# Kernel tuning notes

Hardware: AMD Instinct MI355X
Metric: run time of the kernel (lower is better)

## Reference

```python
import jax, jax.numpy as jnp
import numpy as np

B, L, D = 64, 4096, 512

def setup_inputs() -> dict:
    key = jax.random.key(0)
    k1, k2 = jax.random.split(key)
    current_hidden = jax.random.normal(k1, (B, D), dtype=jnp.float32)
    encoder_outputs = jax.random.normal(k2, (B, L, D), dtype=jnp.float32)
    return {"current_hidden": current_hidden, "encoder_outputs": encoder_outputs}

def reference(current_hidden, encoder_outputs):
    # energy[b, l] = <current_hidden[b], encoder_outputs[b, l]>  (fused batched matmul,
    # replacing the per-timestep python loop of tiny bmms)
    energy = jnp.einsum('bd,bld->bl', current_hidden, encoder_outputs)
    # softmax over the source-length axis (nn.Softmax(dim=1))
    alignment = jax.nn.softmax(energy, axis=1)  # [B, L]
    # context = mean over L of alignment[..., None] * encoder_outputs
    # (original uses torch.mean, i.e. weighted sum divided by L)
    L_ = encoder_outputs.shape[1]
    context = jnp.einsum('bl,bld->bd', alignment, encoder_outputs) / L_
    return context
```

## Files before the change

### kernel.cpp

```cpp
#include <hip/hip_runtime.h>
#include <hip/hip_bf16.h>


#define D_DIM 512
#define B_DIM 64
#define L_DIM 4096

__global__ __launch_bounds__(256) void attn_pass1(
    const float* __restrict__ h,
    const float* __restrict__ enc,
    float* __restrict__ part_ms,
    float* __restrict__ part_ctx,
    int Cblk)
{
    const int b    = blockIdx.y;
    const int c    = blockIdx.x;
    const int tid  = threadIdx.x;
    const int wave = tid >> 6;
    const int lane = tid & 63;

    const int rowsPerBlock = L_DIM / Cblk;
    const int rowsPerWave  = rowsPerBlock >> 2;
    const int l0 = c * rowsPerBlock + wave * rowsPerWave;

    const float4* h4 = reinterpret_cast<const float4*>(h + (size_t)b * D_DIM);
    const float4 h0 = h4[lane];
    const float4 h1 = h4[lane + 64];

    const float* rowp = enc + ((size_t)b * L_DIM + (size_t)l0) * D_DIM + 4 * lane;

    float m = -3.0e38f;
    float s = 0.0f;
    float4 a0 = {0.f, 0.f, 0.f, 0.f};
    float4 a1 = {0.f, 0.f, 0.f, 0.f};

    float4 v0 = *reinterpret_cast<const float4*>(rowp);
    float4 v1 = *reinterpret_cast<const float4*>(rowp + 256);

    for (int r = 0; r < rowsPerWave; ++r) {
        const float* np = rowp + ((r + 1 < rowsPerWave) ? D_DIM : 0);
        const float4 nv0 = *reinterpret_cast<const float4*>(np);
        const float4 nv1 = *reinterpret_cast<const float4*>(np + 256);

        float e = h0.x * v0.x + h0.y * v0.y + h0.z * v0.z + h0.w * v0.w
                + h1.x * v1.x + h1.y * v1.y + h1.z * v1.z + h1.w * v1.w;
        #pragma unroll
        for (int off = 32; off > 0; off >>= 1)
            e += __shfl_xor(e, off, 64);
        if (e > m) {
            const float alpha = __expf(m - e);
            s *= alpha;
            a0.x *= alpha; a0.y *= alpha; a0.z *= alpha; a0.w *= alpha;
            a1.x *= alpha; a1.y *= alpha; a1.z *= alpha; a1.w *= alpha;
            m = e;
        }
        const float w = __expf(e - m);
        s += w;
        a0.x += w * v0.x; a0.y += w * v0.y; a0.z += w * v0.z; a0.w += w * v0.w;
        a1.x += w * v1.x; a1.y += w * v1.y; a1.z += w * v1.z; a1.w += w * v1.w;

        v0 = nv0; v1 = nv1;
        rowp += D_DIM;
    }

    __shared__ float sm_m[4];
    __shared__ float sm_s[4];
    __shared__ float sm_ctx[4][D_DIM];

    reinterpret_cast<float4*>(&sm_ctx[wave][0])[lane]   = a0;
    reinterpret_cast<float4*>(&sm_ctx[wave][256])[lane] = a1;
    if (lane == 0) { sm_m[wave] = m; sm_s[wave] = s; }
    __syncthreads();

    const float M  = fmaxf(fmaxf(sm_m[0], sm_m[1]), fmaxf(sm_m[2], sm_m[3]));
    const float w0 = __expf(sm_m[0] - M);
    const float w1 = __expf(sm_m[1] - M);
    const float w2 = __expf(sm_m[2] - M);
    const float w3 = __expf(sm_m[3] - M);

    if (tid == 0) {
        const float S = sm_s[0] * w0 + sm_s[1] * w1 + sm_s[2] * w2 + sm_s[3] * w3;
        float* ms = part_ms + ((size_t)b * Cblk + c) * 2;
        ms[0] = M;
        ms[1] = S;
    }

    float* dst = part_ctx + ((size_t)b * Cblk + c) * D_DIM;
    for (int d = tid; d < D_DIM; d += 256) {
        dst[d] = sm_ctx[0][d] * w0 + sm_ctx[1][d] * w1
               + sm_ctx[2][d] * w2 + sm_ctx[3][d] * w3;
    }
}

__global__ __launch_bounds__(256) void attn_pass2(
    const float* __restrict__ part_ms,
    const float* __restrict__ part_ctx,
    float* __restrict__ out,
    int Cblk, float invL)
{
    const int b   = blockIdx.x;
    const int tid = threadIdx.x;

    __shared__ float w_sm[64];
    __shared__ float invSL;

    if (tid == 0) {
        const float* ms = part_ms + (size_t)b * Cblk * 2;
        float M = -3.0e38f;
        for (int i = 0; i < Cblk; ++i) M = fmaxf(M, ms[2 * i]);
        float S = 0.f;
        for (int i = 0; i < Cblk; ++i) {
            const float w = __expf(ms[2 * i] - M);
            w_sm[i] = w;
            S += w * ms[2 * i + 1];
        }
        invSL = invL / S;
    }
    __syncthreads();

    const float scale = invSL;
    for (int d = tid; d < D_DIM; d += 256) {
        float acc = 0.f;
        for (int i = 0; i < Cblk; ++i)
            acc += w_sm[i] * part_ctx[((size_t)b * Cblk + i) * D_DIM + d];
        out[(size_t)b * D_DIM + d] = acc * scale;
    }
}

extern "C" void kernel_launch(void* const* d_in, const int* in_sizes, int n_in,
                              void* d_out, int out_size, void* d_ws, size_t ws_size,
                              hipStream_t stream) {
    const float* h   = (const float*)d_in[0];
    const float* enc = (const float*)d_in[1];
    float* out = (float*)d_out;

    int C = 16;
    while (C > 1) {
        const size_t need = ((size_t)B_DIM * C * 2 + (size_t)B_DIM * C * D_DIM) * sizeof(float);
        if (need <= ws_size) break;
        C >>= 1;
    }

    float* part_ms  = (float*)d_ws;
    float* part_ctx = part_ms + (size_t)B_DIM * C * 2;

    dim3 grid1(C, B_DIM);
    attn_pass1<<<grid1, 256, 0, stream>>>(h, enc, part_ms, part_ctx, C);
    attn_pass2<<<B_DIM, 256, 0, stream>>>(part_ms, part_ctx, out, C, 1.0f / (float)L_DIM);
}
```

Before: 678.4 us.

## Fuse two-pass attention into one cooperative kernel with grid sync and atomics

Replaces the partial-result pass plus reduction pass with a single cooperative kernel. Each block writes its local max and sum into the output buffer as scratch, grid-syncs, computes a global rescale factor, then has chunk 0 store and the other chunks atomically add their scaled context into the output. This removes the second launch and the workspace round-trip. In exchange it adds three grid-wide barriers and atomic contention, and it includes a single-block-per-batch fallback in case the cooperative launch fails.

```diff
diff --git a/kernel.cpp b/kernel.cpp
--- a/kernel.cpp
+++ b/kernel.cpp
@@ -1,17 +1,24 @@
 #include <hip/hip_runtime.h>
-#include <hip/hip_bf16.h>
+#include <hip/hip_cooperative_groups.h>
+
+namespace cg = cooperative_groups;
 
 
 #define D_DIM 512
 #define B_DIM 64
 #define L_DIM 4096
-
-__global__ __launch_bounds__(256) void attn_pass1(
+#define CCHUNK 16
+
+__device__ __forceinline__ float dot8(const float4 h0, const float4 h1,
+                                      const float4 v0, const float4 v1) {
+    return h0.x * v0.x + h0.y * v0.y + h0.z * v0.z + h0.w * v0.w
+         + h1.x * v1.x + h1.y * v1.y + h1.z * v1.z + h1.w * v1.w;
+}
+
+__global__ __launch_bounds__(256) void attn_fused_coop(
     const float* __restrict__ h,
     const float* __restrict__ enc,
-    float* __restrict__ part_ms,
-    float* __restrict__ part_ctx,
-    int Cblk)
+    float* __restrict__ out)
 {
     const int b    = blockIdx.y;
     const int c    = blockIdx.x;
@@ -19,8 +26,8 @@
     const int wave = tid >> 6;
     const int lane = tid & 63;
 
-    const int rowsPerBlock = L_DIM / Cblk;
-    const int rowsPerWave  = rowsPerBlock >> 2;
+    constexpr int rowsPerBlock = L_DIM / CCHUNK;
+    constexpr int rowsPerWave  = rowsPerBlock / 4;
     const int l0 = c * rowsPerBlock + wave * rowsPerWave;
 
     const float4* h4 = reinterpret_cast<const float4*>(h + (size_t)b * D_DIM);
@@ -42,8 +49,7 @@
         const float4 nv0 = *reinterpret_cast<const float4*>(np);
         const float4 nv1 = *reinterpret_cast<const float4*>(np + 256);
 
-        float e = h0.x * v0.x + h0.y * v0.y + h0.z * v0.z + h0.w * v0.w
-                + h1.x * v1.x + h1.y * v1.y + h1.z * v1.z + h1.w * v1.w;
+        float e = dot8(h0, h1, v0, v1);
         #pragma unroll
         for (int off = 32; off > 0; off >>= 1)
             e += __shfl_xor(e, off, 64);
@@ -72,58 +78,133 @@
     if (lane == 0) { sm_m[wave] = m; sm_s[wave] = s; }
     __syncthreads();
 
-    const float M  = fmaxf(fmaxf(sm_m[0], sm_m[1]), fmaxf(sm_m[2], sm_m[3]));
-    const float w0 = __expf(sm_m[0] - M);
-    const float w1 = __expf(sm_m[1] - M);
-    const float w2 = __expf(sm_m[2] - M);
-    const float w3 = __expf(sm_m[3] - M);
-
+    const float blkM = fmaxf(fmaxf(sm_m[0], sm_m[1]), fmaxf(sm_m[2], sm_m[3]));
+    const float w0 = __expf(sm_m[0] - blkM);
+    const float w1 = __expf(sm_m[1] - blkM);
+    const float w2 = __expf(sm_m[2] - blkM);
+    const float w3 = __expf(sm_m[3] - blkM);
+
+    for (int d = tid; d < D_DIM; d += 256) {
+        sm_ctx[0][d] = sm_ctx[0][d] * w0 + sm_ctx[1][d] * w1
+                     + sm_ctx[2][d] * w2 + sm_ctx[3][d] * w3;
+    }
     if (tid == 0) {
-        const float S = sm_s[0] * w0 + sm_s[1] * w1 + sm_s[2] * w2 + sm_s[3] * w3;
-        float* ms = part_ms + ((size_t)b * Cblk + c) * 2;
-        ms[0] = M;
-        ms[1] = S;
-    }
-
-    float* dst = part_ctx + ((size_t)b * Cblk + c) * D_DIM;
-    for (int d = tid; d < D_DIM; d += 256) {
-        dst[d] = sm_ctx[0][d] * w0 + sm_ctx[1][d] * w1
-               + sm_ctx[2][d] * w2 + sm_ctx[3][d] * w3;
-    }
-}
-
-__global__ __launch_bounds__(256) void attn_pass2(
-    const float* __restrict__ part_ms,
-    const float* __restrict__ part_ctx,
-    float* __restrict__ out,
-    int Cblk, float invL)
+        const float blkS = sm_s[0] * w0 + sm_s[1] * w1 + sm_s[2] * w2 + sm_s[3] * w3;
+        float* scratch = out + (size_t)(b * CCHUNK + c) * 2;
+        scratch[0] = blkM;
+        scratch[1] = blkS;
+    }
+
+    cg::grid_group g = cg::this_grid();
+    g.sync();
+
+    __shared__ float s_scale;
+    if (tid == 0) {
+        float M = -3.0e38f;
+        #pragma unroll
+        for (int i = 0; i < CCHUNK; ++i)
+            M = fmaxf(M, out[(size_t)(b * CCHUNK + i) * 2]);
+        float S = 0.f;
+        #pragma unroll
+        for (int i = 0; i < CCHUNK; ++i)
+            S += out[(size_t)(b * CCHUNK + i) * 2 + 1]
+               * __expf(out[(size_t)(b * CCHUNK + i) * 2] - M);
+        s_scale = __expf(blkM - M) / (S * (float)L_DIM);
+    }
+    __syncthreads();
+    const float scale = s_scale;
+
+    g.sync();
+
+    if (c == 0) {
+        for (int d = tid; d < D_DIM; d += 256)
+            out[(size_t)b * D_DIM + d] = scale * sm_ctx[0][d];
+    }
+    g.sync();
+    if (c != 0) {
+        for (int d = tid; d < D_DIM; d += 256)
+            atomicAdd(&out[(size_t)b * D_DIM + d], scale * sm_ctx[0][d]);
+    }
+}
+
+__global__ __launch_bounds__(1024) void attn_fallback(
+    const float* __restrict__ h,
+    const float* __restrict__ enc,
+    float* __restrict__ out)
 {
-    const int b   = blockIdx.x;
-    const int tid = threadIdx.x;
-
-    __shared__ float w_sm[64];
-    __shared__ float invSL;
-
-    if (tid == 0) {
-        const float* ms = part_ms + (size_t)b * Cblk * 2;
-        float M = -3.0e38f;
-        for (int i = 0; i < Cblk; ++i) M = fmaxf(M, ms[2 * i]);
-        float S = 0.f;
-        for (int i = 0; i < Cblk; ++i) {
-            const float w = __expf(ms[2 * i] - M);
-            w_sm[i] = w;
-            S += w * ms[2 * i + 1];
+    const int b    = blockIdx.x;
+    const int tid  = threadIdx.x;
+    const int wave = tid >> 6;
+    const int lane = tid & 63;
+
+    constexpr int rowsPerWave = L_DIM / 16;
+    const int l0 = wave * rowsPerWave;
+
+    const float4* h4 = reinterpret_cast<const float4*>(h + (size_t)b * D_DIM);
+    const float4 h0 = h4[lane];
+    const float4 h1 = h4[lane + 64];
+
+    const float* rowp = enc + ((size_t)b * L_DIM + (size_t)l0) * D_DIM + 4 * lane;
+
+    float m = -3.0e38f;
+    float s = 0.0f;
+    float4 a0 = {0.f, 0.f, 0.f, 0.f};
+    float4 a1 = {0.f, 0.f, 0.f, 0.f};
+
+    float4 v0 = *reinterpret_cast<const float4*>(rowp);
+    float4 v1 = *reinterpret_cast<const float4*>(rowp + 256);
+
+    for (int r = 0; r < rowsPerWave; ++r) {
+        const float* np = rowp + ((r + 1 < rowsPerWave) ? D_DIM : 0);
+        const float4 nv0 = *reinterpret_cast<const float4*>(np);
+        const float4 nv1 = *reinterpret_cast<const float4*>(np + 256);
+
+        float e = dot8(h0, h1, v0, v1);
+        #pragma unroll
+        for (int off = 32; off > 0; off >>= 1)
+            e += __shfl_xor(e, off, 64);
+        if (e > m) {
+            const float alpha = __expf(m - e);
+            s *= alpha;
+            a0.x *= alpha; a0.y *= alpha; a0.z *= alpha; a0.w *= alpha;
+            a1.x *= alpha; a1.y *= alpha; a1.z *= alpha; a1.w *= alpha;
+            m = e;
         }
-        invSL = invL / S;
-    }
+        const float w = __expf(e - m);
+        s += w;
+        a0.x += w * v0.x; a0.y += w * v0.y; a0.z += w * v0.z; a0.w += w * v0.w;
+        a1.x += w * v1.x; a1.y += w * v1.y; a1.z += w * v1.z; a1.w += w * v1.w;
+
+        v0 = nv0; v1 = nv1;
+        rowp += D_DIM;
+    }
+
+    __shared__ float sm_m[16];
+    __shared__ float sm_s[16];
+    __shared__ float sm_ctx[16][D_DIM];
+
+    reinterpret_cast<float4*>(&sm_ctx[wave][0])[lane]   = a0;
+    reinterpret_cast<float4*>(&sm_ctx[wave][256])[lane] = a1;
+    if (lane == 0) { sm_m[wave] = m; sm_s[wave] = s; }
     __syncthreads();
 
-    const float scale = invSL;
-    for (int d = tid; d < D_DIM; d += 256) {
+    float M = -3.0e38f;
+    #pragma unroll
+    for (int i = 0; i < 16; ++i) M = fmaxf(M, sm_m[i]);
+    float w[16];
+    float S = 0.f;
+    #pragma unroll
+    for (int i = 0; i < 16; ++i) {
+        w[i] = __expf(sm_m[i] - M);
+        S += sm_s[i] * w[i];
+    }
+    const float inv = 1.0f / (S * (float)L_DIM);
+
+    for (int d = tid; d < D_DIM; d += 1024) {
         float acc = 0.f;
-        for (int i = 0; i < Cblk; ++i)
-            acc += w_sm[i] * part_ctx[((size_t)b * Cblk + i) * D_DIM + d];
-        out[(size_t)b * D_DIM + d] = acc * scale;
+        #pragma unroll
+        for (int i = 0; i < 16; ++i) acc += sm_ctx[i][d] * w[i];
+        out[(size_t)b * D_DIM + d] = acc * inv;
     }
 }
 
@@ -134,17 +215,12 @@
     const float* enc = (const float*)d_in[1];
     float* out = (float*)d_out;
 
-    int C = 16;
-    while (C > 1) {
-        const size_t need = ((size_t)B_DIM * C * 2 + (size_t)B_DIM * C * D_DIM) * sizeof(float);
-        if (need <= ws_size) break;
-        C >>= 1;
-    }
-
-    float* part_ms  = (float*)d_ws;
-    float* part_ctx = part_ms + (size_t)B_DIM * C * 2;
-
-    dim3 grid1(C, B_DIM);
-    attn_pass1<<<grid1, 256, 0, stream>>>(h, enc, part_ms, part_ctx, C);
-    attn_pass2<<<B_DIM, 256, 0, stream>>>(part_ms, part_ctx, out, C, 1.0f / (float)L_DIM);
-}
+    void* args[] = { (void*)&h, (void*)&enc, (void*)&out };
+    hipError_t err = hipLaunchCooperativeKernel(
+        reinterpret_cast<const void*>(&attn_fused_coop),
+        dim3(CCHUNK, B_DIM), dim3(256), args, 0, stream);
+
+    if (err != hipSuccess) {
+        attn_fallback<<<B_DIM, 1024, 0, stream>>>(h, enc, out);
+    }
+}
```

Result: slower. 986.7 us (+45.4%).

## Interleave rows across waves and double chunk count for more parallelism

Applied to the files above, without the earlier changes.

Doubles the number of chunks per batch to 32, which makes the first-pass grid twice as large, and adds an occupancy hint to launch bounds. Rows are now assigned to waves with an interleaved stride, so concurrently running waves read adjacent rows instead of contiguous private ranges. The intent is to fill more of the GPU and improve DRAM locality on this memory-bound kernel. The workspace-size fallback is removed, so the code now assumes the workspace always fits 32 partials per batch.

```diff
diff --git a/kernel.cpp b/kernel.cpp
--- a/kernel.cpp
+++ b/kernel.cpp
@@ -1,33 +1,33 @@
 #include <hip/hip_runtime.h>
-#include <hip/hip_bf16.h>
 
 
 #define D_DIM 512
 #define B_DIM 64
 #define L_DIM 4096
+#define C_CHUNK 32
+#define WPB 4
+#define WAVES_PER_B (C_CHUNK * WPB)
+#define ROWS_PER_WAVE (L_DIM / WAVES_PER_B)
 
-__global__ __launch_bounds__(256) void attn_pass1(
+__global__ __launch_bounds__(256, 8) void attn_pass1i(
     const float* __restrict__ h,
     const float* __restrict__ enc,
     float* __restrict__ part_ms,
-    float* __restrict__ part_ctx,
-    int Cblk)
+    float* __restrict__ part_ctx)
 {
     const int b    = blockIdx.y;
     const int c    = blockIdx.x;
     const int tid  = threadIdx.x;
     const int wave = tid >> 6;
     const int lane = tid & 63;
-
-    const int rowsPerBlock = L_DIM / Cblk;
-    const int rowsPerWave  = rowsPerBlock >> 2;
-    const int l0 = c * rowsPerBlock + wave * rowsPerWave;
+    const int g    = c * WPB + wave;
 
     const float4* h4 = reinterpret_cast<const float4*>(h + (size_t)b * D_DIM);
     const float4 h0 = h4[lane];
     const float4 h1 = h4[lane + 64];
 
-    const float* rowp = enc + ((size_t)b * L_DIM + (size_t)l0) * D_DIM + 4 * lane;
+    const float* rowp = enc + ((size_t)b * L_DIM + (size_t)g) * D_DIM + 4 * lane;
+    const size_t rowStride = (size_t)WAVES_PER_B * D_DIM;
 
     float m = -3.0e38f;
     float s = 0.0f;
@@ -37,8 +37,8 @@
     float4 v0 = *reinterpret_cast<const float4*>(rowp);
     float4 v1 = *reinterpret_cast<const float4*>(rowp + 256);
 
-    for (int r = 0; r < rowsPerWave; ++r) {
-        const float* np = rowp + ((r + 1 < rowsPerWave) ? D_DIM : 0);
+    for (int r = 0; r < ROWS_PER_WAVE; ++r) {
+        const float* np = rowp + ((r + 1 < ROWS_PER_WAVE) ? rowStride : 0);
         const float4 nv0 = *reinterpret_cast<const float4*>(np);
         const float4 nv1 = *reinterpret_cast<const float4*>(np + 256);
 
@@ -60,7 +60,7 @@
         a1.x += w * v1.x; a1.y += w * v1.y; a1.z += w * v1.z; a1.w += w * v1.w;
 
         v0 = nv0; v1 = nv1;
-        rowp += D_DIM;
+        rowp += rowStride;
     }
 
     __shared__ float sm_m[4];
@@ -80,12 +80,12 @@
 
     if (tid == 0) {
         const float S = sm_s[0] * w0 + sm_s[1] * w1 + sm_s[2] * w2 + sm_s[3] * w3;
-        float* ms = part_ms + ((size_t)b * Cblk + c) * 2;
+        float* ms = part_ms + ((size_t)b * C_CHUNK + c) * 2;
         ms[0] = M;
         ms[1] = S;
     }
 
-    float* dst = part_ctx + ((size_t)b * Cblk + c) * D_DIM;
+    float* dst = part_ctx + ((size_t)b * C_CHUNK + c) * D_DIM;
     for (int d = tid; d < D_DIM; d += 256) {
         dst[d] = sm_ctx[0][d] * w0 + sm_ctx[1][d] * w1
                + sm_ctx[2][d] * w2 + sm_ctx[3][d] * w3;
@@ -96,20 +96,20 @@
     const float* __restrict__ part_ms,
     const float* __restrict__ part_ctx,
     float* __restrict__ out,
-    int Cblk, float invL)
+    float invL)
 {
     const int b   = blockIdx.x;
     const int tid = threadIdx.x;
 
-    __shared__ float w_sm[64];
+    __shared__ float w_sm[C_CHUNK];
     __shared__ float invSL;
 
     if (tid == 0) {
-        const float* ms = part_ms + (size_t)b * Cblk * 2;
+        const float* ms = part_ms + (size_t)b * C_CHUNK * 2;
         float M = -3.0e38f;
-        for (int i = 0; i < Cblk; ++i) M = fmaxf(M, ms[2 * i]);
+        for (int i = 0; i < C_CHUNK; ++i) M = fmaxf(M, ms[2 * i]);
         float S = 0.f;
-        for (int i = 0; i < Cblk; ++i) {
+        for (int i = 0; i < C_CHUNK; ++i) {
             const float w = __expf(ms[2 * i] - M);
             w_sm[i] = w;
             S += w * ms[2 * i + 1];
@@ -121,8 +121,9 @@
     const float scale = invSL;
     for (int d = tid; d < D_DIM; d += 256) {
         float acc = 0.f;
-        for (int i = 0; i < Cblk; ++i)
-            acc += w_sm[i] * part_ctx[((size_t)b * Cblk + i) * D_DIM + d];
+        #pragma unroll 8
+        for (int i = 0; i < C_CHUNK; ++i)
+            acc += w_sm[i] * part_ctx[((size_t)b * C_CHUNK + i) * D_DIM + d];
         out[(size_t)b * D_DIM + d] = acc * scale;
     }
 }
@@ -134,17 +135,11 @@
     const float* enc = (const float*)d_in[1];
     float* out = (float*)d_out;
 
-    int C = 16;
-    while (C > 1) {
-        const size_t need = ((size_t)B_DIM * C * 2 + (size_t)B_DIM * C * D_DIM) * sizeof(float);
-        if (need <= ws_size) break;
-        C >>= 1;
-    }
+    float* part_ms  = (float*)d_ws;
+    float* part_ctx = part_ms + (size_t)B_DIM * C_CHUNK * 2;
 
-    float* part_ms  = (float*)d_ws;
-    float* part_ctx = part_ms + (size_t)B_DIM * C * 2;
-
-    dim3 grid1(C, B_DIM);
-    attn_pass1<<<grid1, 256, 0, stream>>>(h, enc, part_ms, part_ctx, C);
-    attn_pass2<<<B_DIM, 256, 0, stream>>>(part_ms, part_ctx, out, C, 1.0f / (float)L_DIM);
+    dim3 grid1(C_CHUNK, B_DIM);
+    attn_pass1i<<<grid1, 256, 0, stream>>>(h, enc, part_ms, part_ctx);
+    attn_pass2<<<B_DIM, 256, 0, stream>>>(part_ms, part_ctx, out,
+                                          1.0f / (float)L_DIM);
 }
```

Result: no change. 689.8 us (+1.7%).
